# Kernel optimization log

Measured on AMD Instinct MI355X. Metric: run time of the kernel, lower is better.

## Reference

```python
import jax, jax.numpy as jnp
import numpy as np

B, T, F, H, A, D = 1024, 256, 128, 128, 8, 256


def setup_inputs() -> dict:
    key = jax.random.key(0)
    ks = jax.random.split(key, 16)
    s = lambda k, shape, scale: jax.random.normal(k, shape, dtype=jnp.float32) * scale
    return {
        "h": jax.random.normal(ks[0], (B, T, F), dtype=jnp.float32),
        # LSTM params (flax LSTMCell: input kernel no bias, hidden kernel with bias; gate order i,f,g,o)
        "Wx": s(ks[1], (F, 4 * H), 1.0 / np.sqrt(F)),
        "Wh": s(ks[2], (H, 4 * H), 1.0 / np.sqrt(H)),
        "bh": jnp.zeros((4 * H,), jnp.float32),
        # actor head
        "Wa1": s(ks[3], (H, D), np.sqrt(2.0 / H)),
        "ba1": jnp.zeros((D,), jnp.float32),
        "Wa2": s(ks[4], (D, D), np.sqrt(2.0 / D)),
        "ba2": jnp.zeros((D,), jnp.float32),
        "Wa3": s(ks[5], (D, A), 0.01 / np.sqrt(D)),
        "ba3": jnp.zeros((A,), jnp.float32),
        "log_std": jnp.zeros((A,), jnp.float32),
        # critic head
        "Wc1": s(ks[6], (H, D), np.sqrt(2.0 / H)),
        "bc1": jnp.zeros((D,), jnp.float32),
        "Wc2": s(ks[7], (D, D), np.sqrt(2.0 / D)),
        "bc2": jnp.zeros((D,), jnp.float32),
        "Wc3": s(ks[8], (D, 1), 1.0 / np.sqrt(D)),
        "bc3": jnp.zeros((1,), jnp.float32),
    }


def reference(h, Wx, Wh, bh, Wa1, ba1, Wa2, ba2, Wa3, ba3, log_std,
              Wc1, bc1, Wc2, bc2, Wc3, bc3):
    act = jnp.tanh  # activation='tanh'
    # Precompute input projections for all gates: [B,T,4H] -> scan over time.
    xg = jnp.einsum('btf,fg->btg', h, Wx)
    c0 = jnp.zeros((h.shape[0], H), h.dtype)
    h0 = jnp.zeros((h.shape[0], H), h.dtype)

    def step(carry, xg_t):
        c, hs = carry
        z = xg_t + hs @ Wh + bh  # [B,4H]
        i = jax.nn.sigmoid(z[:, :H])
        f = jax.nn.sigmoid(z[:, H:2 * H])
        g = jnp.tanh(z[:, 2 * H:3 * H])
        o = jax.nn.sigmoid(z[:, 3 * H:])
        c = f * c + i * g
        hs = o * jnp.tanh(c)
        return (c, hs), None

    (_, x), _ = jax.lax.scan(step, (c0, h0), jnp.swapaxes(xg, 0, 1))  # x = last hidden [B,H]

    a = act(x @ Wa1 + ba1)
    a = act(a @ Wa2 + ba2)
    mean = a @ Wa3 + ba3                      # [B,A] policy mean
    std = jnp.exp(log_std)                    # [A] policy std (diag)

    v = act(x @ Wc1 + bc1)
    v = act(v @ Wc2 + bc2)
    value = (v @ Wc3 + bc3)                   # [B,1]

    # Pack (mean, std, value) as in (pi, critic): [B, 2A+1]
    return jnp.concatenate([mean, jnp.broadcast_to(std, mean.shape), value], axis=-1)
```

## Files before the change

### kernel.cpp

```cpp
#include <hip/hip_runtime.h>


typedef _Float16 f16x8 __attribute__((ext_vector_type(8)));
typedef _Float16 f16x4 __attribute__((ext_vector_type(4)));
typedef float    f32x4 __attribute__((ext_vector_type(4)));

#define NLOG2E (-1.4426950408889634f)

__device__ __forceinline__ float rcpf(float x) { return __builtin_amdgcn_rcpf(x); }
__device__ __forceinline__ float ex2(float x)  { return __builtin_amdgcn_exp2f(x); }

__device__ __forceinline__ f16x4 pack4(const float4 a) {
    f16x4 v;
    v[0] = (_Float16)a.x; v[1] = (_Float16)a.y;
    v[2] = (_Float16)a.z; v[3] = (_Float16)a.w;
    return v;
}

__global__ __launch_bounds__(512, 2)
void ac_fused(const float* __restrict__ hin,
              const float* __restrict__ Wx, const float* __restrict__ Wh,
              const float* __restrict__ bh,
              const float* __restrict__ Wa1, const float* __restrict__ ba1,
              const float* __restrict__ Wa2, const float* __restrict__ ba2,
              const float* __restrict__ Wa3, const float* __restrict__ ba3,
              const float* __restrict__ logstd,
              const float* __restrict__ Wc1, const float* __restrict__ bc1,
              const float* __restrict__ Wc2, const float* __restrict__ bc2,
              const float* __restrict__ Wc3, const float* __restrict__ bc3,
              float* __restrict__ out)
{
    constexpr int T = 256, F = 128, H = 128, G = 512;

    __shared__ f16x8 Hbuf[2][16][4];
    __shared__ f16x8 Axg[2][256];
    __shared__ float xf[4][F + 1];
    __shared__ float hb1[2][4][257];
    __shared__ float hb2[2][4][257];
    __shared__ float redA[4][8][8];
    __shared__ float redC[4][32];

    const int tid  = threadIdx.x;
    const int lane = tid & 63;
    const int wv   = tid >> 6;
    const int m16  = lane & 15;
    const int q    = lane >> 4;
    const int r0   = blockIdx.x << 2;
    const int ncol = (wv << 4) + m16;

    f16x8 bwx[4][4], bwh[4][4];
    #pragma unroll
    for (int kt = 0; kt < 4; ++kt) {
        #pragma unroll
        for (int s = 0; s < 4; ++s) {
            f16x8 vx, vh;
            #pragma unroll
            for (int j = 0; j < 8; ++j) {
                const int k = (kt << 5) + (q << 3) + j;
                vx[j] = (_Float16)Wx[k * G + s * H + ncol];
                vh[j] = (_Float16)Wh[k * G + s * H + ncol];
            }
            bwx[s][kt] = vx;
            bwh[s][kt] = vh;
        }
    }
    const float nbi = NLOG2E * bh[0 * H + ncol];
    const float nbf = NLOG2E * bh[1 * H + ncol];
    const float nbg = 2.0f * NLOG2E * bh[2 * H + ncol];
    const float nbo = NLOG2E * bh[3 * H + ncol];

    const f32x4 zq = {0.f, 0.f, 0.f, 0.f};

    const int xc = tid >> 1;
    const int xh = tid & 1;
    const int xk0 = ((xc >> 6) << 5) + (((xc >> 4) & 3) << 3) + (xh << 2);
    const float* pgbase = hin + (size_t)(r0 + ((xc >> 2) & 3)) * T * F
                              + (size_t)(xc & 3) * F + xk0;

    const int hr0 = (q << 2) + (m16 >> 2);
    const int hw  = ((((ncol >> 3) << 2) + q) << 3) + (ncol & 7);

    if (tid < 128) {
        f16x8 zz = {};
        ((f16x8*)Hbuf)[tid] = zz;
    }

    {
        const float4 xp0 = *(const float4*)(pgbase);
        const float4 xp1 = *(const float4*)(pgbase + 4 * (size_t)F);
        __syncthreads();
        *(f16x4*)((_Float16*)&Axg[0][0] + xc * 8 + xh * 4) = pack4(xp0);
        *(f16x4*)((_Float16*)&Axg[1][0] + xc * 8 + xh * 4) = pack4(xp1);
    }
    asm volatile("s_waitcnt lgkmcnt(0)" ::: "memory");
    __builtin_amdgcn_s_barrier();

    float cstate = 0.0f;
    float hcur   = 0.0f;

    for (int t0 = 0; t0 < T; t0 += 8) {
        f32x4 P[2][4];
        {
            const f16x8 fr0 = Axg[0][lane];
            const f16x8 fr1 = Axg[1][lane];
            P[0][0] = __builtin_amdgcn_mfma_f32_16x16x32_f16(fr0, bwx[0][0], zq, 0, 0, 0);
            P[0][1] = __builtin_amdgcn_mfma_f32_16x16x32_f16(fr0, bwx[1][0], zq, 0, 0, 0);
            P[0][2] = __builtin_amdgcn_mfma_f32_16x16x32_f16(fr0, bwx[2][0], zq, 0, 0, 0);
            P[0][3] = __builtin_amdgcn_mfma_f32_16x16x32_f16(fr0, bwx[3][0], zq, 0, 0, 0);
            P[1][0] = __builtin_amdgcn_mfma_f32_16x16x32_f16(fr1, bwx[0][0], zq, 0, 0, 0);
            P[1][1] = __builtin_amdgcn_mfma_f32_16x16x32_f16(fr1, bwx[1][0], zq, 0, 0, 0);
            P[1][2] = __builtin_amdgcn_mfma_f32_16x16x32_f16(fr1, bwx[2][0], zq, 0, 0, 0);
            P[1][3] = __builtin_amdgcn_mfma_f32_16x16x32_f16(fr1, bwx[3][0], zq, 0, 0, 0);
        }
        #pragma unroll
        for (int kt = 1; kt < 4; ++kt) {
            const f16x8 fr0 = Axg[0][(kt << 6) + lane];
            const f16x8 fr1 = Axg[1][(kt << 6) + lane];
            P[0][0] = __builtin_amdgcn_mfma_f32_16x16x32_f16(fr0, bwx[0][kt], P[0][0], 0, 0, 0);
            P[0][1] = __builtin_amdgcn_mfma_f32_16x16x32_f16(fr0, bwx[1][kt], P[0][1], 0, 0, 0);
            P[0][2] = __builtin_amdgcn_mfma_f32_16x16x32_f16(fr0, bwx[2][kt], P[0][2], 0, 0, 0);
            P[0][3] = __builtin_amdgcn_mfma_f32_16x16x32_f16(fr0, bwx[3][kt], P[0][3], 0, 0, 0);
            P[1][0] = __builtin_amdgcn_mfma_f32_16x16x32_f16(fr1, bwx[0][kt], P[1][0], 0, 0, 0);
            P[1][1] = __builtin_amdgcn_mfma_f32_16x16x32_f16(fr1, bwx[1][kt], P[1][1], 0, 0, 0);
            P[1][2] = __builtin_amdgcn_mfma_f32_16x16x32_f16(fr1, bwx[2][kt], P[1][2], 0, 0, 0);
            P[1][3] = __builtin_amdgcn_mfma_f32_16x16x32_f16(fr1, bwx[3][kt], P[1][3], 0, 0, 0);
        }
        #pragma unroll
        for (int mt = 0; mt < 2; ++mt) {
            #pragma unroll
            for (int g = 0; g < 4; ++g) {
                P[mt][0][g] = fmaf(P[mt][0][g], NLOG2E,        nbi);
                P[mt][1][g] = fmaf(P[mt][1][g], NLOG2E,        nbf);
                P[mt][2][g] = fmaf(P[mt][2][g], 2.0f * NLOG2E, nbg);
                P[mt][3][g] = fmaf(P[mt][3][g], NLOG2E,        nbo);
            }
        }

        float4 xp0n, xp1n;
        #pragma unroll
        for (int i = 0; i < 8; ++i) {
            const int t = t0 + i;
            const f16x8* Hc = &Hbuf[t & 1][0][0];
            _Float16*    Hn = (_Float16*)&Hbuf[(t + 1) & 1][0][0];

            const f16x8 af0 = Hc[hr0];
            const f16x8 af1 = Hc[16 + hr0];
            const f16x8 af2 = Hc[32 + hr0];
            const f16x8 af3 = Hc[48 + hr0];

            if (i == 2) {
                const int t0n = (t0 + 8 < T) ? t0 + 8 : t0;
                xp0n = *(const float4*)(pgbase + (size_t)t0n * F);
                xp1n = *(const float4*)(pgbase + (size_t)(t0n + 4) * F);
            }

            f32x4 a0 = __builtin_amdgcn_mfma_f32_16x16x32_f16(af0, bwh[0][0], zq, 0, 0, 0);
            f32x4 a1 = __builtin_amdgcn_mfma_f32_16x16x32_f16(af0, bwh[1][0], zq, 0, 0, 0);
            f32x4 a2 = __builtin_amdgcn_mfma_f32_16x16x32_f16(af0, bwh[2][0], zq, 0, 0, 0);
            f32x4 a3 = __builtin_amdgcn_mfma_f32_16x16x32_f16(af0, bwh[3][0], zq, 0, 0, 0);
            a0 = __builtin_amdgcn_mfma_f32_16x16x32_f16(af1, bwh[0][1], a0, 0, 0, 0);
            a1 = __builtin_amdgcn_mfma_f32_16x16x32_f16(af1, bwh[1][1], a1, 0, 0, 0);
            a2 = __builtin_amdgcn_mfma_f32_16x16x32_f16(af1, bwh[2][1], a2, 0, 0, 0);
            a3 = __builtin_amdgcn_mfma_f32_16x16x32_f16(af1, bwh[3][1], a3, 0, 0, 0);
            a0 = __builtin_amdgcn_mfma_f32_16x16x32_f16(af2, bwh[0][2], a0, 0, 0, 0);
            a1 = __builtin_amdgcn_mfma_f32_16x16x32_f16(af2, bwh[1][2], a1, 0, 0, 0);
            a2 = __builtin_amdgcn_mfma_f32_16x16x32_f16(af2, bwh[2][2], a2, 0, 0, 0);
            a3 = __builtin_amdgcn_mfma_f32_16x16x32_f16(af2, bwh[3][2], a3, 0, 0, 0);
            a0 = __builtin_amdgcn_mfma_f32_16x16x32_f16(af3, bwh[0][3], a0, 0, 0, 0);
            a1 = __builtin_amdgcn_mfma_f32_16x16x32_f16(af3, bwh[1][3], a1, 0, 0, 0);
            a2 = __builtin_amdgcn_mfma_f32_16x16x32_f16(af3, bwh[2][3], a2, 0, 0, 0);
            a3 = __builtin_amdgcn_mfma_f32_16x16x32_f16(af3, bwh[3][3], a3, 0, 0, 0);

            const int mt = i >> 2, rg = i & 3;
            const float iv = rcpf(1.0f + ex2(fmaf(a0[0], NLOG2E,        P[mt][0][rg])));
            const float fv = rcpf(1.0f + ex2(fmaf(a1[0], NLOG2E,        P[mt][1][rg])));
            const float gv = 2.0f * rcpf(1.0f + ex2(fmaf(a2[0], 2.0f * NLOG2E, P[mt][2][rg]))) - 1.0f;
            const float ov = rcpf(1.0f + ex2(fmaf(a3[0], NLOG2E,        P[mt][3][rg])));
            cstate = fv * cstate + iv * gv;
            const float th = 2.0f * rcpf(1.0f + ex2(cstate * (2.0f * NLOG2E))) - 1.0f;
            hcur = ov * th;

            Hn[hw] = (_Float16)hcur;

            if (i == 7) {
                *(f16x4*)((_Float16*)&Axg[0][0] + xc * 8 + xh * 4) = pack4(xp0n);
                *(f16x4*)((_Float16*)&Axg[1][0] + xc * 8 + xh * 4) = pack4(xp1n);
            }

            asm volatile("s_waitcnt lgkmcnt(0)" ::: "memory");
            __builtin_amdgcn_s_barrier();
        }
    }

    xf[q][ncol] = hcur;
    __syncthreads();

    const int half = tid >> 8;
    const int n    = tid & 255;
    const float* W1 = half ? Wc1 : Wa1;
    const float* b1 = half ? bc1 : ba1;
    const float* W2 = half ? Wc2 : Wa2;
    const float* b2 = half ? bc2 : ba2;

    auto tanhl = [&](float x) { return 2.0f * rcpf(1.0f + ex2(x * (2.0f * NLOG2E))) - 1.0f; };

    {
        float a0, a1, a2, a3;
        const float b = b1[n];
        a0 = a1 = a2 = a3 = b;
        #pragma unroll 16
        for (int k = 0; k < 128; ++k) {
            const float w = W1[k * 256 + n];
            a0 += xf[0][k] * w; a1 += xf[1][k] * w;
            a2 += xf[2][k] * w; a3 += xf[3][k] * w;
        }
        hb1[half][0][n] = tanhl(a0); hb1[half][1][n] = tanhl(a1);
        hb1[half][2][n] = tanhl(a2); hb1[half][3][n] = tanhl(a3);
    }
    __syncthreads();
    {
        float a0, a1, a2, a3;
        const float b = b2[n];
        a0 = a1 = a2 = a3 = b;
        #pragma unroll 16
        for (int k = 0; k < 256; ++k) {
            const float w = W2[k * 256 + n];
            a0 += hb1[half][0][k] * w; a1 += hb1[half][1][k] * w;
            a2 += hb1[half][2][k] * w; a3 += hb1[half][3][k] * w;
        }
        hb2[half][0][n] = tanhl(a0); hb2[half][1][n] = tanhl(a1);
        hb2[half][2][n] = tanhl(a2); hb2[half][3][n] = tanhl(a3);
    }
    __syncthreads();
    if (tid < 256) {
        const int r = tid >> 6, aa = (tid >> 3) & 7, seg = tid & 7;
        float acc = 0.0f;
        const int k0 = seg << 5;
        #pragma unroll 16
        for (int k = k0; k < k0 + 32; ++k) acc += hb2[0][r][k] * Wa3[k * 8 + aa];
        redA[r][aa][seg] = acc;
    } else if (tid < 384) {
        const int u = tid - 256;
        const int r = u >> 5, seg = u & 31;
        float acc = 0.0f;
        const int k0 = seg << 3;
        #pragma unroll
        for (int k = k0; k < k0 + 8; ++k) acc += hb2[1][r][k] * Wc3[k];
        redC[r][seg] = acc;
    }
    __syncthreads();
    if (tid < 32) {
        const int r = tid >> 3, aa = tid & 7;
        float acc = ba3[aa];
        #pragma unroll
        for (int s = 0; s < 8; ++s) acc += redA[r][aa][s];
        out[(size_t)(r0 + r) * 17 + aa]     = acc;
        out[(size_t)(r0 + r) * 17 + 8 + aa] = __expf(logstd[aa]);
    } else if (tid >= 64 && tid < 68) {
        const int r = tid - 64;
        float acc = bc3[0];
        #pragma unroll
        for (int s = 0; s < 32; ++s) acc += redC[r][s];
        out[(size_t)(r0 + r) * 17 + 16] = acc;
    }
}

extern "C" void kernel_launch(void* const* d_in, const int* in_sizes, int n_in,
                              void* d_out, int out_size, void* d_ws, size_t ws_size,
                              hipStream_t stream) {
    (void)in_sizes; (void)n_in; (void)d_ws; (void)ws_size; (void)out_size;
    const float* hin = (const float*)d_in[0];
    const float* Wx  = (const float*)d_in[1];
    const float* Wh  = (const float*)d_in[2];
    const float* bh  = (const float*)d_in[3];
    const float* Wa1 = (const float*)d_in[4];
    const float* ba1 = (const float*)d_in[5];
    const float* Wa2 = (const float*)d_in[6];
    const float* ba2 = (const float*)d_in[7];
    const float* Wa3 = (const float*)d_in[8];
    const float* ba3 = (const float*)d_in[9];
    const float* ls  = (const float*)d_in[10];
    const float* Wc1 = (const float*)d_in[11];
    const float* bc1 = (const float*)d_in[12];
    const float* Wc2 = (const float*)d_in[13];
    const float* bc2 = (const float*)d_in[14];
    const float* Wc3 = (const float*)d_in[15];
    const float* bc3 = (const float*)d_in[16];

    hipLaunchKernelGGL(ac_fused, dim3(256), dim3(512), 0, stream,
                       hin, Wx, Wh, bh, Wa1, ba1, Wa2, ba2, Wa3, ba3, ls,
                       Wc1, bc1, Wc2, bc2, Wc3, bc3, (float*)d_out);
}
```

Baseline: 342.2 us.

## Shrink input-projection chunk to 4 steps and split recurrent MFMA chains

The per-chunk input projection now covers 4 timesteps instead of 8, halving the Axg staging buffer and the P register set. The recurrent Wh matmul is split into two independent accumulation chains per gate (k-tiles 0-1 and 2-3) that are summed afterward. The gate sigmoids for i and f are issued before the g and o MFMAs so their transcendental math can overlap with the remaining matrix work. The aim is shorter dependent MFMA latency on the serial critical path and lower register pressure. In exchange, input-projection MFMAs are issued twice as often and there are extra adds.

Measured after the change: 356.1 us. 1.04x slower.

```diff
diff --git a/kernel.cpp b/kernel.cpp
--- a/kernel.cpp
+++ b/kernel.cpp
@@ -33,7 +33,7 @@
     constexpr int T = 256, F = 128, H = 128, G = 512;
 
     __shared__ f16x8 Hbuf[2][16][4];
-    __shared__ f16x8 Axg[2][256];
+    __shared__ f16x8 Axg[256];
     __shared__ float xf[4][F + 1];
     __shared__ float hb1[2][4][257];
     __shared__ float hb2[2][4][257];
@@ -87,10 +87,8 @@
 
     {
         const float4 xp0 = *(const float4*)(pgbase);
-        const float4 xp1 = *(const float4*)(pgbase + 4 * (size_t)F);
         __syncthreads();
-        *(f16x4*)((_Float16*)&Axg[0][0] + xc * 8 + xh * 4) = pack4(xp0);
-        *(f16x4*)((_Float16*)&Axg[1][0] + xc * 8 + xh * 4) = pack4(xp1);
+        *(f16x4*)((_Float16*)&Axg[0] + xc * 8 + xh * 4) = pack4(xp0);
     }
     asm volatile("s_waitcnt lgkmcnt(0)" ::: "memory");
     __builtin_amdgcn_s_barrier();
@@ -98,93 +96,75 @@
     float cstate = 0.0f;
     float hcur   = 0.0f;
 
-    for (int t0 = 0; t0 < T; t0 += 8) {
-        f32x4 P[2][4];
+    for (int t0 = 0; t0 < T; t0 += 4) {
+        f32x4 P[4];
         {
-            const f16x8 fr0 = Axg[0][lane];
-            const f16x8 fr1 = Axg[1][lane];
-            P[0][0] = __builtin_amdgcn_mfma_f32_16x16x32_f16(fr0, bwx[0][0], zq, 0, 0, 0);
-            P[0][1] = __builtin_amdgcn_mfma_f32_16x16x32_f16(fr0, bwx[1][0], zq, 0, 0, 0);
-            P[0][2] = __builtin_amdgcn_mfma_f32_16x16x32_f16(fr0, bwx[2][0], zq, 0, 0, 0);
-            P[0][3] = __builtin_amdgcn_mfma_f32_16x16x32_f16(fr0, bwx[3][0], zq, 0, 0, 0);
-            P[1][0] = __builtin_amdgcn_mfma_f32_16x16x32_f16(fr1, bwx[0][0], zq, 0, 0, 0);
-            P[1][1] = __builtin_amdgcn_mfma_f32_16x16x32_f16(fr1, bwx[1][0], zq, 0, 0, 0);
-            P[1][2] = __builtin_amdgcn_mfma_f32_16x16x32_f16(fr1, bwx[2][0], zq, 0, 0, 0);
-            P[1][3] = __builtin_amdgcn_mfma_f32_16x16x32_f16(fr1, bwx[3][0], zq, 0, 0, 0);
+            const f16x8 fr = Axg[lane];
+            P[0] = __builtin_amdgcn_mfma_f32_16x16x32_f16(fr, bwx[0][0], zq, 0, 0, 0);
+            P[1] = __builtin_amdgcn_mfma_f32_16x16x32_f16(fr, bwx[1][0], zq, 0, 0, 0);
+            P[2] = __builtin_amdgcn_mfma_f32_16x16x32_f16(fr, bwx[2][0], zq, 0, 0, 0);
+            P[3] = __builtin_amdgcn_mfma_f32_16x16x32_f16(fr, bwx[3][0], zq, 0, 0, 0);
         }
         #pragma unroll
         for (int kt = 1; kt < 4; ++kt) {
-            const f16x8 fr0 = Axg[0][(kt << 6) + lane];
-            const f16x8 fr1 = Axg[1][(kt << 6) + lane];
-            P[0][0] = __builtin_amdgcn_mfma_f32_16x16x32_f16(fr0, bwx[0][kt], P[0][0], 0, 0, 0);
-            P[0][1] = __builtin_amdgcn_mfma_f32_16x16x32_f16(fr0, bwx[1][kt], P[0][1], 0, 0, 0);
-            P[0][2] = __builtin_amdgcn_mfma_f32_16x16x32_f16(fr0, bwx[2][kt], P[0][2], 0, 0, 0);
-            P[0][3] = __builtin_amdgcn_mfma_f32_16x16x32_f16(fr0, bwx[3][kt], P[0][3], 0, 0, 0);
-            P[1][0] = __builtin_amdgcn_mfma_f32_16x16x32_f16(fr1, bwx[0][kt], P[1][0], 0, 0, 0);
-            P[1][1] = __builtin_amdgcn_mfma_f32_16x16x32_f16(fr1, bwx[1][kt], P[1][1], 0, 0, 0);
-            P[1][2] = __builtin_amdgcn_mfma_f32_16x16x32_f16(fr1, bwx[2][kt], P[1][2], 0, 0, 0);
-            P[1][3] = __builtin_amdgcn_mfma_f32_16x16x32_f16(fr1, bwx[3][kt], P[1][3], 0, 0, 0);
-        }
-        #pragma unroll
-        for (int mt = 0; mt < 2; ++mt) {
-            #pragma unroll
-            for (int g = 0; g < 4; ++g) {
-                P[mt][0][g] = fmaf(P[mt][0][g], NLOG2E,        nbi);
-                P[mt][1][g] = fmaf(P[mt][1][g], NLOG2E,        nbf);
-                P[mt][2][g] = fmaf(P[mt][2][g], 2.0f * NLOG2E, nbg);
-                P[mt][3][g] = fmaf(P[mt][3][g], NLOG2E,        nbo);
-            }
-        }
-
-        float4 xp0n, xp1n;
-        #pragma unroll
-        for (int i = 0; i < 8; ++i) {
-            const int t = t0 + i;
-            const f16x8* Hc = &Hbuf[t & 1][0][0];
-            _Float16*    Hn = (_Float16*)&Hbuf[(t + 1) & 1][0][0];
+            const f16x8 fr = Axg[(kt << 6) + lane];
+            P[0] = __builtin_amdgcn_mfma_f32_16x16x32_f16(fr, bwx[0][kt], P[0], 0, 0, 0);
+            P[1] = __builtin_amdgcn_mfma_f32_16x16x32_f16(fr, bwx[1][kt], P[1], 0, 0, 0);
+            P[2] = __builtin_amdgcn_mfma_f32_16x16x32_f16(fr, bwx[2][kt], P[2], 0, 0, 0);
+            P[3] = __builtin_amdgcn_mfma_f32_16x16x32_f16(fr, bwx[3][kt], P[3], 0, 0, 0);
+        }
+        P[0] = P[0] * NLOG2E          + f32x4{nbi, nbi, nbi, nbi};
+        P[1] = P[1] * NLOG2E          + f32x4{nbf, nbf, nbf, nbf};
+        P[2] = P[2] * (2.0f * NLOG2E) + f32x4{nbg, nbg, nbg, nbg};
+        P[3] = P[3] * NLOG2E          + f32x4{nbo, nbo, nbo, nbo};
+
+        float4 xpn;
+        #pragma unroll
+        for (int i = 0; i < 4; ++i) {
+            const f16x8* Hc = &Hbuf[i & 1][0][0];
+            _Float16*    Hn = (_Float16*)&Hbuf[(i + 1) & 1][0][0];
 
             const f16x8 af0 = Hc[hr0];
             const f16x8 af1 = Hc[16 + hr0];
             const f16x8 af2 = Hc[32 + hr0];
             const f16x8 af3 = Hc[48 + hr0];
 
-            if (i == 2) {
-                const int t0n = (t0 + 8 < T) ? t0 + 8 : t0;
-                xp0n = *(const float4*)(pgbase + (size_t)t0n * F);
-                xp1n = *(const float4*)(pgbase + (size_t)(t0n + 4) * F);
+            if (i == 1) {
+                const int t0n = (t0 + 4 < T) ? t0 + 4 : t0;
+                xpn = *(const float4*)(pgbase + (size_t)t0n * F);
             }
 
-            f32x4 a0 = __builtin_amdgcn_mfma_f32_16x16x32_f16(af0, bwh[0][0], zq, 0, 0, 0);
-            f32x4 a1 = __builtin_amdgcn_mfma_f32_16x16x32_f16(af0, bwh[1][0], zq, 0, 0, 0);
-            f32x4 a2 = __builtin_amdgcn_mfma_f32_16x16x32_f16(af0, bwh[2][0], zq, 0, 0, 0);
-            f32x4 a3 = __builtin_amdgcn_mfma_f32_16x16x32_f16(af0, bwh[3][0], zq, 0, 0, 0);
-            a0 = __builtin_amdgcn_mfma_f32_16x16x32_f16(af1, bwh[0][1], a0, 0, 0, 0);
-            a1 = __builtin_amdgcn_mfma_f32_16x16x32_f16(af1, bwh[1][1], a1, 0, 0, 0);
-            a2 = __builtin_amdgcn_mfma_f32_16x16x32_f16(af1, bwh[2][1], a2, 0, 0, 0);
-            a3 = __builtin_amdgcn_mfma_f32_16x16x32_f16(af1, bwh[3][1], a3, 0, 0, 0);
-            a0 = __builtin_amdgcn_mfma_f32_16x16x32_f16(af2, bwh[0][2], a0, 0, 0, 0);
-            a1 = __builtin_amdgcn_mfma_f32_16x16x32_f16(af2, bwh[1][2], a1, 0, 0, 0);
-            a2 = __builtin_amdgcn_mfma_f32_16x16x32_f16(af2, bwh[2][2], a2, 0, 0, 0);
-            a3 = __builtin_amdgcn_mfma_f32_16x16x32_f16(af2, bwh[3][2], a3, 0, 0, 0);
-            a0 = __builtin_amdgcn_mfma_f32_16x16x32_f16(af3, bwh[0][3], a0, 0, 0, 0);
-            a1 = __builtin_amdgcn_mfma_f32_16x16x32_f16(af3, bwh[1][3], a1, 0, 0, 0);
-            a2 = __builtin_amdgcn_mfma_f32_16x16x32_f16(af3, bwh[2][3], a2, 0, 0, 0);
-            a3 = __builtin_amdgcn_mfma_f32_16x16x32_f16(af3, bwh[3][3], a3, 0, 0, 0);
-
-            const int mt = i >> 2, rg = i & 3;
-            const float iv = rcpf(1.0f + ex2(fmaf(a0[0], NLOG2E,        P[mt][0][rg])));
-            const float fv = rcpf(1.0f + ex2(fmaf(a1[0], NLOG2E,        P[mt][1][rg])));
-            const float gv = 2.0f * rcpf(1.0f + ex2(fmaf(a2[0], 2.0f * NLOG2E, P[mt][2][rg]))) - 1.0f;
-            const float ov = rcpf(1.0f + ex2(fmaf(a3[0], NLOG2E,        P[mt][3][rg])));
+            f32x4 ci0 = __builtin_amdgcn_mfma_f32_16x16x32_f16(af0, bwh[0][0], zq, 0, 0, 0);
+            f32x4 ci1 = __builtin_amdgcn_mfma_f32_16x16x32_f16(af2, bwh[0][2], zq, 0, 0, 0);
+            f32x4 cf0 = __builtin_amdgcn_mfma_f32_16x16x32_f16(af0, bwh[1][0], zq, 0, 0, 0);
+            f32x4 cf1 = __builtin_amdgcn_mfma_f32_16x16x32_f16(af2, bwh[1][2], zq, 0, 0, 0);
+            ci0 = __builtin_amdgcn_mfma_f32_16x16x32_f16(af1, bwh[0][1], ci0, 0, 0, 0);
+            ci1 = __builtin_amdgcn_mfma_f32_16x16x32_f16(af3, bwh[0][3], ci1, 0, 0, 0);
+            cf0 = __builtin_amdgcn_mfma_f32_16x16x32_f16(af1, bwh[1][1], cf0, 0, 0, 0);
+            cf1 = __builtin_amdgcn_mfma_f32_16x16x32_f16(af3, bwh[1][3], cf1, 0, 0, 0);
+
+            const float iv = rcpf(1.0f + ex2(fmaf(ci0[0] + ci1[0], NLOG2E, P[0][i])));
+            const float fv = rcpf(1.0f + ex2(fmaf(cf0[0] + cf1[0], NLOG2E, P[1][i])));
+
+            f32x4 cg0 = __builtin_amdgcn_mfma_f32_16x16x32_f16(af0, bwh[2][0], zq, 0, 0, 0);
+            f32x4 cg1 = __builtin_amdgcn_mfma_f32_16x16x32_f16(af2, bwh[2][2], zq, 0, 0, 0);
+            f32x4 co0 = __builtin_amdgcn_mfma_f32_16x16x32_f16(af0, bwh[3][0], zq, 0, 0, 0);
+            f32x4 co1 = __builtin_amdgcn_mfma_f32_16x16x32_f16(af2, bwh[3][2], zq, 0, 0, 0);
+            cg0 = __builtin_amdgcn_mfma_f32_16x16x32_f16(af1, bwh[2][1], cg0, 0, 0, 0);
+            cg1 = __builtin_amdgcn_mfma_f32_16x16x32_f16(af3, bwh[2][3], cg1, 0, 0, 0);
+            co0 = __builtin_amdgcn_mfma_f32_16x16x32_f16(af1, bwh[3][1], co0, 0, 0, 0);
+            co1 = __builtin_amdgcn_mfma_f32_16x16x32_f16(af3, bwh[3][3], co1, 0, 0, 0);
+
+            const float gv = 2.0f * rcpf(1.0f + ex2(fmaf(cg0[0] + cg1[0], 2.0f * NLOG2E, P[2][i]))) - 1.0f;
+            const float ov = rcpf(1.0f + ex2(fmaf(co0[0] + co1[0], NLOG2E, P[3][i])));
             cstate = fv * cstate + iv * gv;
             const float th = 2.0f * rcpf(1.0f + ex2(cstate * (2.0f * NLOG2E))) - 1.0f;
             hcur = ov * th;
 
             Hn[hw] = (_Float16)hcur;
 
-            if (i == 7) {
-                *(f16x4*)((_Float16*)&Axg[0][0] + xc * 8 + xh * 4) = pack4(xp0n);
-                *(f16x4*)((_Float16*)&Axg[1][0] + xc * 8 + xh * 4) = pack4(xp1n);
+            if (i == 3) {
+                *(f16x4*)((_Float16*)&Axg[0] + xc * 8 + xh * 4) = pack4(xpn);
             }
 
             asm volatile("s_waitcnt lgkmcnt(0)" ::: "memory");
```
